# Optimization experiments

Measured on AMD Instinct MI355X. Metric: run time of the kernel, lower is better.

The kernel has to match this reference:

```python
import jax, jax.numpy as jnp
import numpy as np

LAYER_NUM = 2
NUM_CLS = 128
HIDDEN = 256
NUM_NODES = 1024


def setup_inputs() -> dict:
    key = jax.random.key(0)
    ks = jax.random.split(key, 12)
    s = 0.05
    return {
        "x": jax.random.normal(ks[0], (NUM_NODES, HIDDEN), jnp.float32),
        "knowledge": jax.random.uniform(ks[1], (NUM_CLS, NUM_CLS), jnp.float32) / NUM_CLS,
        "w3w": jax.random.normal(ks[2], (HIDDEN, 2 * HIDDEN), jnp.float32) * s,
        "b3w": jax.random.normal(ks[3], (HIDDEN,), jnp.float32) * s,
        "u3": jax.random.normal(ks[4], (HIDDEN, HIDDEN), jnp.float32) * s,
        "bu3": jax.random.normal(ks[5], (HIDDEN,), jnp.float32) * s,
        "w4w": jax.random.normal(ks[6], (HIDDEN, 2 * HIDDEN), jnp.float32) * s,
        "b4w": jax.random.normal(ks[7], (HIDDEN,), jnp.float32) * s,
        "w5w": jax.random.normal(ks[8], (HIDDEN, 2 * HIDDEN), jnp.float32) * s,
        "b5w": jax.random.normal(ks[9], (HIDDEN,), jnp.float32) * s,
        "u5": jax.random.normal(ks[10], (HIDDEN, HIDDEN), jnp.float32) * s,
        "bu5": jax.random.normal(ks[11], (HIDDEN,), jnp.float32) * s,
    }


def reference(x, knowledge, w3w, b3w, u3, bu3, w4w, b4w, w5w, b5w, u5, bu5):
    N, H = x.shape
    C = knowledge.shape[0]
    # hidden[n, c, :] = x[n, :]  (repeat per class)
    hidden = jnp.broadcast_to(x[:, None, :], (N, C, H))
    for _ in range(LAYER_NUM):
        hs = hidden.sum(0)                      # [C, H]
        diff = hs[None, :, :] - hidden          # [N, C, H]
        # knowledge.T @ diff_n  and  knowledge @ diff_n, vectorized over nodes
        left = jnp.einsum('kc,nkh->nch', knowledge, diff)
        right = jnp.einsum('ck,nkh->nch', knowledge, diff)
        av = jnp.concatenate([left, right], axis=-1).reshape(N * C, 2 * H)
        h = hidden.reshape(N * C, H)
        uh3 = h @ u3.T + bu3                    # shared: rv uses fc_eq3_u (source quirk)
        zv = jax.nn.sigmoid(av @ w3w.T + b3w + uh3)
        rv = jax.nn.sigmoid(av @ w4w.T + b4w + uh3)
        hv = jnp.tanh(av @ w5w.T + b5w + (rv * h) @ u5.T + bu5)
        h = (1.0 - zv) * h + zv * hv
        hidden = h.reshape(N, C, H)
    return hidden
```

## Files before the change

kernel.cpp:

```cpp
#include <hip/hip_runtime.h>
#include <cstdint>
#include <cstddef>


#define NODES 1024
#define NCLS  128
#define HID   256

using frag  = __attribute__((ext_vector_type(8))) short;
using frag4 = __attribute__((ext_vector_type(4))) short;
using f32x4 = __attribute__((ext_vector_type(4))) float;

__device__ __forceinline__ float bf2f(unsigned short h){
  unsigned int u = ((unsigned int)h) << 16;
  float f; __builtin_memcpy(&f, &u, 4); return f;
}
__device__ __forceinline__ unsigned short f2bf(float f){
  unsigned int u; __builtin_memcpy(&u, &f, 4);
  u = (u + 0x7fffu + ((u >> 16) & 1u)) >> 16;
  return (unsigned short)u;
}
__device__ __forceinline__ float sigm(float x){ return 1.0f/(1.0f + __expf(-x)); }
__device__ __forceinline__ float tanh_fast(float x){ return 1.0f - 2.0f/(__expf(2.0f*x) + 1.0f); }

#define GLOBAL_AS(p) ((const __attribute__((address_space(1))) void*)(p))
#define LDS_AS(p)    ((__attribute__((address_space(3))) void*)(p))

template<int OUT_BF16>
__global__ __launch_bounds__(256) void gemm_bf16(
    const unsigned short* __restrict__ A0, int ldA0, int K0,
    const unsigned short* __restrict__ A1, int ldA1,
    const unsigned short* __restrict__ BT, int ldB, long bStride,
    void* __restrict__ Cptr, int ldC,
    int Ntiles, int Ktot, unsigned int aMask, int Mtiles)
{
  __shared__ unsigned short As[4096];
  __shared__ unsigned short Bs[4096];
  const int t   = threadIdx.x;
  const int bid = blockIdx.x;
  const int xcd = bid & 7, slot = bid >> 3;
  const int mtPerX = (Mtiles >= 8) ? (Mtiles >> 3) : 1;
  const int mt = xcd * mtPerX + slot / Ntiles;
  const int nt = slot % Ntiles;
  const int lane = t & 63, w = t >> 6;
  const int wm = w >> 1, wn = w & 1;
  const int r = lane & 15, q = lane >> 4;
  const int m0 = mt * 128, n0 = nt * 128;
  const unsigned short* Bbase = BT + (size_t)mt * (size_t)bStride;

  f32x4 acc[4][4] = {};

  for (int kb = 0; kb < Ktot; kb += 32) {
#pragma unroll
    for (int i = 0; i < 2; ++i) {
      int u  = i * 256 + t;
      int mi = u >> 2;
      int kc = (u & 3) * 8;
      int k  = kb + kc;
      const unsigned short* ga;
      if (k < K0) ga = A0 + (size_t)((unsigned int)(m0 + mi) & aMask) * (size_t)ldA0 + k;
      else        ga = A1 + (size_t)(m0 + mi) * (size_t)ldA1 + (k - K0);
      __builtin_amdgcn_global_load_lds(GLOBAL_AS(ga), LDS_AS(&As[u * 8]), 16, 0, 0);
      const unsigned short* gb = Bbase + (size_t)(n0 + mi) * (size_t)ldB + k;
      __builtin_amdgcn_global_load_lds(GLOBAL_AS(gb), LDS_AS(&Bs[u * 8]), 16, 0, 0);
    }
    __syncthreads();

    frag af[4], bf_[4];
#pragma unroll
    for (int x = 0; x < 4; ++x) {
      af[x]  = *(const frag*)&As[(wm * 64 + x * 16 + r) * 32 + q * 8];
      bf_[x] = *(const frag*)&Bs[(wn * 64 + x * 16 + r) * 32 + q * 8];
    }
#pragma unroll
    for (int x = 0; x < 4; ++x)
#pragma unroll
      for (int y = 0; y < 4; ++y)
        acc[x][y] = __builtin_amdgcn_mfma_f32_16x16x32_bf16(af[x], bf_[y], acc[x][y], 0, 0, 0);
    __syncthreads();
  }

#pragma unroll
  for (int x = 0; x < 4; ++x) {
#pragma unroll
    for (int y = 0; y < 4; ++y) {
      int col = n0 + wn * 64 + y * 16 + r;
#pragma unroll
      for (int g = 0; g < 4; ++g) {
        long row = m0 + wm * 64 + x * 16 + q * 4 + g;
        if (OUT_BF16) ((unsigned short*)Cptr)[row * (long)ldC + col] = f2bf(acc[x][y][g]);
        else          ((float*)Cptr)[row * (long)ldC + col] = acc[x][y][g];
      }
    }
  }
}

__global__ __launch_bounds__(256, 4) void gemm_pre(
    const unsigned short* __restrict__ AVH, const unsigned short* __restrict__ H1,
    const unsigned short* __restrict__ WB, unsigned short* __restrict__ PRE)
{
  __shared__ unsigned short As[8192];
  __shared__ unsigned short Bs[8192];
  const int t   = threadIdx.x;
  const int bid = blockIdx.x;
  const int xcd = bid & 7, slot = bid >> 3;
  const int mt = xcd * 128 + slot / 6;
  const int ct = slot % 6;
  const int lane = t & 63, w = t >> 6;
  const int wm = w >> 1, wn = w & 1;
  const int r = lane & 15, q = lane >> 4;
  const int m0 = mt * 128;
  const unsigned short* Wrow = WB + (size_t)(ct * 128) * 768;

  f32x4 acc[4][4] = {};

  for (int kb = 0; kb < 512; kb += 64) {
#pragma unroll
    for (int i = 0; i < 4; ++i) {
      int u  = i * 256 + t;
      int mi = u >> 3;
      int gc = (u & 7) ^ (mi & 7);
      __builtin_amdgcn_global_load_lds(GLOBAL_AS(AVH + (size_t)(m0 + mi) * 512 + kb + gc * 8),
                                       LDS_AS(&As[u * 8]), 16, 0, 0);
      __builtin_amdgcn_global_load_lds(GLOBAL_AS(Wrow + (size_t)mi * 768 + kb + gc * 8),
                                       LDS_AS(&Bs[u * 8]), 16, 0, 0);
    }
    __syncthreads();
#pragma unroll
    for (int kh = 0; kh < 2; ++kh) {
      frag af[4], bf_[4];
#pragma unroll
      for (int x = 0; x < 4; ++x) {
        int ra = wm * 64 + x * 16 + r;
        int rb = wn * 64 + x * 16 + r;
        af[x]  = *(const frag*)&As[ra * 64 + (((kh * 4 + q) ^ (ra & 7)) * 8)];
        bf_[x] = *(const frag*)&Bs[rb * 64 + (((kh * 4 + q) ^ (rb & 7)) * 8)];
      }
#pragma unroll
      for (int x = 0; x < 4; ++x)
#pragma unroll
        for (int y = 0; y < 4; ++y)
          acc[x][y] = __builtin_amdgcn_mfma_f32_16x16x32_bf16(af[x], bf_[y], acc[x][y], 0, 0, 0);
    }
    __syncthreads();
  }

  if (ct < 4) {
    for (int kb = 0; kb < 256; kb += 64) {
#pragma unroll
      for (int i = 0; i < 4; ++i) {
        int u  = i * 256 + t;
        int mi = u >> 3;
        int gc = (u & 7) ^ (mi & 7);
        __builtin_amdgcn_global_load_lds(GLOBAL_AS(H1 + (size_t)(m0 + mi) * 256 + kb + gc * 8),
                                         LDS_AS(&As[u * 8]), 16, 0, 0);
        __builtin_amdgcn_global_load_lds(GLOBAL_AS(Wrow + (size_t)mi * 768 + 512 + kb + gc * 8),
                                         LDS_AS(&Bs[u * 8]), 16, 0, 0);
      }
      __syncthreads();
#pragma unroll
      for (int kh = 0; kh < 2; ++kh) {
        frag af[4], bf_[4];
#pragma unroll
        for (int x = 0; x < 4; ++x) {
          int ra = wm * 64 + x * 16 + r;
          int rb = wn * 64 + x * 16 + r;
          af[x]  = *(const frag*)&As[ra * 64 + (((kh * 4 + q) ^ (ra & 7)) * 8)];
          bf_[x] = *(const frag*)&Bs[rb * 64 + (((kh * 4 + q) ^ (rb & 7)) * 8)];
        }
#pragma unroll
        for (int x = 0; x < 4; ++x)
#pragma unroll
          for (int y = 0; y < 4; ++y)
            acc[x][y] = __builtin_amdgcn_mfma_f32_16x16x32_bf16(af[x], bf_[y], acc[x][y], 0, 0, 0);
      }
      __syncthreads();
    }
  }

#pragma unroll
  for (int x = 0; x < 4; ++x) {
#pragma unroll
    for (int y = 0; y < 4; ++y) {
      int col = ct * 128 + wn * 64 + y * 16 + r;
#pragma unroll
      for (int g = 0; g < 4; ++g) {
        long row = m0 + wm * 64 + x * 16 + q * 4 + g;
        PRE[row * 768 + col] = f2bf(acc[x][y][g]);
      }
    }
  }
}

__global__ __launch_bounds__(256) void gemm_l1(
    const float* __restrict__ XW, const float* __restrict__ SW,
    const float* __restrict__ x,
    const float* __restrict__ b3, const float* __restrict__ b4,
    const float* __restrict__ b5, const float* __restrict__ bu3,
    const float* __restrict__ bu5,
    const float* __restrict__ colsum, const float* __restrict__ rowsum,
    const unsigned short* __restrict__ u5b,
    const unsigned short* __restrict__ KTbN, const unsigned short* __restrict__ KbN,
    unsigned short* __restrict__ H1, unsigned short* __restrict__ AVH)
{
  __shared__ unsigned short SM[17408];
  unsigned short* As = SM;
  unsigned short* Bs = SM + 4096;
  unsigned short* L  = SM;
  __shared__ float tP1[256], tP2[256], tP3[256], tX[256];
  __shared__ float tZ1[256], tZ2[256], tZ3[256];
  __shared__ float tV1[256], tV2[256], tV3[256];
  __shared__ float tCS[128], tRS[128];

  const int t = threadIdx.x, bid = blockIdx.x;
  const int xcd = bid & 7, slot = bid >> 3;
  const int n  = xcd * 128 + (slot >> 1);
  const int nt = slot & 1;
  const int lane = t & 63, w = t >> 6, wm = w >> 1, wn = w & 1;
  const int r = lane & 15, q = lane >> 4;
  const int n0 = nt * 128;
  const float* xw = XW + (size_t)n * 1792;

  {
    int i = t;
    float xwi0 = xw[i], xwi1 = xw[256 + i], xwi2 = xw[512 + i], xwi3 = xw[768 + i];
    float xwi4 = xw[1024 + i], xwi5 = xw[1280 + i], xwu = xw[1536 + i];
    tP1[i] = SW[512 + i] - xwi2;
    tP2[i] = SW[768 + i] - xwi3;
    tP3[i] = xwu + b4[i] + bu3[i];
    tX[i]  = x[(size_t)n * HID + i];
    tZ1[i] = SW[i] - xwi0;
    tZ2[i] = SW[256 + i] - xwi1;
    tZ3[i] = xwu + b3[i] + bu3[i];
    tV1[i] = SW[1024 + i] - xwi4;
    tV2[i] = SW[1280 + i] - xwi5;
    tV3[i] = b5[i] + bu5[i];
    if (t < 128) { tCS[t] = colsum[t]; tRS[t] = rowsum[t]; }
  }
  __syncthreads();

  f32x4 acc[4][4] = {};

  for (int kb = 0; kb < 256; kb += 32) {
#pragma unroll
    for (int i = 0; i < 2; ++i) {
      int u  = i * 256 + t;
      int mi = u >> 2;
      int c  = u & 3;
      int kc = c * 8;
      int k  = kb + kc;
      int gc = c ^ (mi & 3);
      __builtin_amdgcn_global_load_lds(GLOBAL_AS(u5b + (size_t)(n0 + mi) * 256 + kb + gc * 8),
                                       LDS_AS(&Bs[u * 8]), 16, 0, 0);
      float cs = tCS[mi], rs = tRS[mi];
      frag a;
#pragma unroll
      for (int e = 0; e < 8; ++e) {
        int i2 = k + e;
        float pre = cs * tP1[i2] + rs * tP2[i2] + tP3[i2];
        a[e] = (short)f2bf(sigm(pre) * tX[i2]);
      }
      *(frag*)&As[mi * 32 + (c ^ (mi & 3)) * 8] = a;
    }
    __syncthreads();

    frag af[4], bf_[4];
#pragma unroll
    for (int xx = 0; xx < 4; ++xx) {
      int ra = wm * 64 + xx * 16 + r;
      int rb = wn * 64 + xx * 16 + r;
      af[xx]  = *(const frag*)&As[ra * 32 + ((q ^ (ra & 3)) * 8)];
      bf_[xx] = *(const frag*)&Bs[rb * 32 + ((q ^ (rb & 3)) * 8)];
    }
#pragma unroll
    for (int xx = 0; xx < 4; ++xx)
#pragma unroll
      for (int y = 0; y < 4; ++y)
        acc[xx][y] = __builtin_amdgcn_mfma_f32_16x16x32_bf16(af[xx], bf_[y], acc[xx][y], 0, 0, 0);
    __syncthreads();
  }

#pragma unroll
  for (int xx = 0; xx < 4; ++xx) {
#pragma unroll
    for (int y = 0; y < 4; ++y) {
      int j = wn * 64 + y * 16 + r;
      int i = n0 + j;
      frag4 pack;
#pragma unroll
      for (int g = 0; g < 4; ++g) {
        int c = wm * 64 + xx * 16 + q * 4 + g;
        float cs = tCS[c], rs = tRS[c];
        float z  = sigm(cs * tZ1[i] + rs * tZ2[i] + tZ3[i]);
        float p5 = cs * tV1[i] + rs * tV2[i] + tV3[i] + acc[xx][y][g];
        float h1 = (1.0f - z) * tX[i] + z * tanh_fast(p5);
        unsigned short hb = f2bf(h1);
        pack[g] = (short)hb;
        H1[(size_t)(n * 128 + c) * HID + i] = hb;
      }
      *(frag4*)&L[j * 136 + (wm * 64 + xx * 16 + q * 4)] = pack;
    }
  }
  __syncthreads();

#pragma unroll
  for (int s = 0; s < 2; ++s) {
    const unsigned short* Ks = s ? KbN : KTbN;
    f32x4 a2[4][4] = {};
#pragma unroll
    for (int kb = 0; kb < 4; ++kb) {
      frag af[4], bf_[4];
#pragma unroll
      for (int xx = 0; xx < 4; ++xx) {
        int cp = wm * 64 + xx * 16 + r;
        af[xx] = *(const frag*)(Ks + (size_t)cp * 128 + kb * 32 + q * 8);
        int j = wn * 64 + xx * 16 + r;
        bf_[xx] = *(const frag*)&L[j * 136 + kb * 32 + q * 8];
      }
#pragma unroll
      for (int xx = 0; xx < 4; ++xx)
#pragma unroll
        for (int y = 0; y < 4; ++y)
          a2[xx][y] = __builtin_amdgcn_mfma_f32_16x16x32_bf16(af[xx], bf_[y], a2[xx][y], 0, 0, 0);
    }
#pragma unroll
    for (int xx = 0; xx < 4; ++xx)
#pragma unroll
      for (int y = 0; y < 4; ++y) {
        int col = s * 256 + n0 + wn * 64 + y * 16 + r;
#pragma unroll
        for (int g = 0; g < 4; ++g) {
          int cp = wm * 64 + xx * 16 + q * 4 + g;
          AVH[(size_t)(n * 128 + cp) * 512 + col] = f2bf(a2[xx][y][g]);
        }
      }
  }
}

__global__ __launch_bounds__(256) void gemm_l2(
    const unsigned short* __restrict__ PRE, const float* __restrict__ SG,
    const unsigned short* __restrict__ H1, const unsigned short* __restrict__ u5b,
    float* __restrict__ out)
{
  __shared__ unsigned short As[4096], Bs[4096];
  const int t = threadIdx.x, bid = blockIdx.x;
  const int xcd = bid & 7, slot = bid >> 3;
  const int mt = xcd * 128 + (slot >> 1);
  const int nt = slot & 1;
  const int lane = t & 63, w = t >> 6, wm = w >> 1, wn = w & 1;
  const int r = lane & 15, q = lane >> 4;
  const int m0 = mt * 128, n0 = nt * 128;

  f32x4 acc[4][4] = {};

  for (int kb = 0; kb < 256; kb += 32) {
#pragma unroll
    for (int i = 0; i < 2; ++i) {
      int u  = i * 256 + t;
      int mi = u >> 2;
      int c  = u & 3;
      int k  = kb + c * 8;
      int gc = c ^ (mi & 3);
      __builtin_amdgcn_global_load_lds(GLOBAL_AS(u5b + (size_t)(n0 + mi) * 256 + kb + gc * 8),
                                       LDS_AS(&Bs[u * 8]), 16, 0, 0);
      long row = m0 + mi;
      frag p4 = *(const frag*)(PRE + row * 768 + 256 + k);
      frag h1 = *(const frag*)(H1 + row * 256 + k);
      const float* sg = SG + (size_t)mi * 768 + 256 + k;
      frag a;
#pragma unroll
      for (int e = 0; e < 8; ++e) {
        float rv = sigm(sg[e] + bf2f((unsigned short)p4[e]));
        a[e] = (short)f2bf(rv * bf2f((unsigned short)h1[e]));
      }
      *(frag*)&As[mi * 32 + (c ^ (mi & 3)) * 8] = a;
    }
    __syncthreads();

    frag af[4], bf_[4];
#pragma unroll
    for (int xx = 0; xx < 4; ++xx) {
      int ra = wm * 64 + xx * 16 + r;
      int rb = wn * 64 + xx * 16 + r;
      af[xx]  = *(const frag*)&As[ra * 32 + ((q ^ (ra & 3)) * 8)];
      bf_[xx] = *(const frag*)&Bs[rb * 32 + ((q ^ (rb & 3)) * 8)];
    }
#pragma unroll
    for (int xx = 0; xx < 4; ++xx)
#pragma unroll
      for (int y = 0; y < 4; ++y)
        acc[xx][y] = __builtin_amdgcn_mfma_f32_16x16x32_bf16(af[xx], bf_[y], acc[xx][y], 0, 0, 0);
    __syncthreads();
  }

#pragma unroll
  for (int xx = 0; xx < 4; ++xx) {
#pragma unroll
    for (int y = 0; y < 4; ++y) {
      int i = n0 + wn * 64 + y * 16 + r;
#pragma unroll
      for (int g = 0; g < 4; ++g) {
        int c = wm * 64 + xx * 16 + q * 4 + g;
        long row = m0 + c;
        float z  = sigm(SG[(size_t)c * 768 + i] + bf2f(PRE[row * 768 + i]));
        float pv = SG[(size_t)c * 768 + 512 + i] + bf2f(PRE[row * 768 + 512 + i])
                 + acc[xx][y][g];
        float h  = bf2f(H1[row * 256 + i]);
        out[row * 256 + i] = (1.0f - z) * h + z * tanh_fast(pv);
      }
    }
  }
}

__global__ __launch_bounds__(256) void prep_cast(
    const float* __restrict__ x, const float* __restrict__ Kn,
    const float* __restrict__ w3, const float* __restrict__ u3,
    const float* __restrict__ w4, const float* __restrict__ w5,
    const float* __restrict__ u5,
    unsigned short* __restrict__ xb, unsigned short* __restrict__ WB,
    unsigned short* __restrict__ WB2, unsigned short* __restrict__ u5b,
    unsigned short* __restrict__ KbN, unsigned short* __restrict__ KTbN)
{
  int idx = blockIdx.x * 256 + threadIdx.x;
  if (idx < 262144) { xb[idx] = f2bf(x[idx]); return; }
  idx -= 262144;
  if (idx < 589824) {
    int col = idx / 768, j = idx % 768;
    int g = col >> 8, i = col & 255;
    float v;
    if (j < 512) { const float* wg = (g == 0) ? w3 : (g == 1) ? w4 : w5; v = wg[(size_t)i * 512 + j]; }
    else v = (g < 2) ? u3[(size_t)i * 256 + (j - 512)] : 0.0f;
    WB[(size_t)col * 768 + j] = f2bf(v);
    return;
  }
  idx -= 589824;
  if (idx < 458752) {
    int col = idx / 256, h = idx % 256;
    int b = col >> 8, i = col & 255;
    float v = (b < 6) ? ((b < 2 ? w3 : (b < 4 ? w4 : w5))[(size_t)i * 512 + (b & 1) * 256 + h])
                      : u3[(size_t)i * 256 + h];
    WB2[(size_t)col * 256 + h] = f2bf(v);
    return;
  }
  idx -= 458752;
  if (idx < 65536) { u5b[idx] = f2bf(u5[idx]); return; }
  idx -= 65536;
  if (idx < 16384) { int c = idx >> 7, k = idx & 127; KbN[idx]  = f2bf(-Kn[c * 128 + k]); return; }
  idx -= 16384;
  { int c = idx >> 7, k = idx & 127; KTbN[idx] = f2bf(-Kn[k * 128 + c]); }
}

__global__ __launch_bounds__(256) void prep_reduce(
    const float* __restrict__ x, const float* __restrict__ Kn,
    float* __restrict__ S, float* __restrict__ colsum, float* __restrict__ rowsum)
{
  int b = blockIdx.x, t = threadIdx.x;
  if (b < 8) {
    float s = 0.f;
    for (int n = 0; n < 128; ++n) s += x[(size_t)(b * 128 + n) * HID + t];
    atomicAdd(&S[t], s);
  } else if (b == 8) {
    if (t < NCLS) { float s = 0.f; for (int k = 0; k < NCLS; ++k) s += Kn[k * NCLS + t]; colsum[t] = s; }
  } else {
    if (t < NCLS) { float s = 0.f; for (int k = 0; k < NCLS; ++k) s += Kn[t * NCLS + k]; rowsum[t] = s; }
  }
}

__global__ __launch_bounds__(256) void prep_sw(
    const float* __restrict__ S, const float* __restrict__ w3,
    const float* __restrict__ w4, const float* __restrict__ w5, float* __restrict__ SW)
{
  int col = blockIdx.x * 256 + threadIdx.x;
  int b = col >> 8, i = col & 255;
  const float* w = (b < 2) ? w3 : (b < 4) ? w4 : w5;
  const float* row = w + (size_t)i * 512 + (b & 1) * 256;
  float s = 0.f;
  for (int h = 0; h < HID; ++h) s += S[h] * row[h];
  SW[col] = s;
}

__global__ __launch_bounds__(256) void reduce_hs(
    const unsigned short* __restrict__ H1, float* __restrict__ hs)
{
  int bid = blockIdx.x;
  int c = bid >> 5, nch = bid & 31;
  int i = threadIdx.x;
  const unsigned short* p = H1 + (size_t)nch * 32 * NCLS * HID + (size_t)c * HID + i;
  float s = 0.f;
  for (int n = 0; n < 32; ++n) s += bf2f(p[(size_t)n * NCLS * HID]);
  atomicAdd(&hs[c * HID + i], s);
}

__global__ __launch_bounds__(256) void p2a(
    const float* __restrict__ hs, const float* __restrict__ w3,
    const float* __restrict__ w4, const float* __restrict__ w5, float* __restrict__ hsW)
{
  __shared__ float hrow[HID];
  int k = blockIdx.x & 127, b = blockIdx.x >> 7;
  int t = threadIdx.x;
  hrow[t] = hs[k * HID + t];
  __syncthreads();
  const float* w = (b < 2) ? w3 : (b < 4) ? w4 : w5;
  const float* row = w + (size_t)t * 512 + (b & 1) * 256;
  float s = 0.f;
  for (int h = 0; h < HID; ++h) s += hrow[h] * row[h];
  hsW[(size_t)k * 1536 + b * 256 + t] = s;
}

__global__ __launch_bounds__(256) void p2b(
    const float* __restrict__ hsW, const float* __restrict__ Kn,
    const float* __restrict__ b3, const float* __restrict__ b4, const float* __restrict__ b5,
    const float* __restrict__ bu3, const float* __restrict__ bu5, float* __restrict__ SG)
{
  __shared__ float kc[NCLS], kr[NCLS];
  int c = blockIdx.x, t = threadIdx.x;
  if (t < NCLS) { kc[t] = Kn[t * NCLS + c]; kr[t] = Kn[c * NCLS + t]; }
  __syncthreads();
  for (int g = 0; g < 3; ++g) {
    int i = t;
    const float* L = hsW + (size_t)(2 * g) * 256 + i;
    const float* R = hsW + (size_t)(2 * g + 1) * 256 + i;
    float s = 0.f;
    for (int k = 0; k < NCLS; ++k) s += kc[k] * L[(size_t)k * 1536] + kr[k] * R[(size_t)k * 1536];
    const float* bg = (g == 0) ? b3 : (g == 1) ? b4 : b5;
    s += bg[i] + ((g < 2) ? bu3[i] : bu5[i]);
    SG[(size_t)c * 768 + g * 256 + i] = s;
  }
}

extern "C" void kernel_launch(void* const* d_in, const int* in_sizes, int n_in,
                              void* d_out, int out_size, void* d_ws, size_t ws_size,
                              hipStream_t stream) {
  (void)in_sizes; (void)n_in; (void)out_size; (void)ws_size;
  const float* x   = (const float*)d_in[0];
  const float* Kn  = (const float*)d_in[1];
  const float* w3  = (const float*)d_in[2];
  const float* b3  = (const float*)d_in[3];
  const float* u3  = (const float*)d_in[4];
  const float* bu3 = (const float*)d_in[5];
  const float* w4  = (const float*)d_in[6];
  const float* b4  = (const float*)d_in[7];
  const float* w5  = (const float*)d_in[8];
  const float* b5  = (const float*)d_in[9];
  const float* u5  = (const float*)d_in[10];
  const float* bu5 = (const float*)d_in[11];
  float* out = (float*)d_out;

  char* w = (char*)d_ws;
  unsigned short* AVH = (unsigned short*)(w);
  unsigned short* PRE = (unsigned short*)(w + 134217728);
  unsigned short* H1  = (unsigned short*)(w + 335544320);
  float*          XW  = (float*)(w + 402653184);
  char* misc = w + 409993216;
  float* S      = (float*)(misc);
  float* hs     = (float*)(misc + 1024);
  float* SW     = (float*)(misc + 132096);
  float* colsum = (float*)(misc + 138240);
  float* rowsum = (float*)(misc + 138752);
  float* hsW    = (float*)(misc + 139264);
  float* SG     = (float*)(misc + 925696);
  unsigned short* WB   = (unsigned short*)(misc + 1318912);
  unsigned short* WB2  = (unsigned short*)(misc + 2498560);
  unsigned short* u5b  = (unsigned short*)(misc + 3416064);
  unsigned short* KbN  = (unsigned short*)(misc + 3547136);
  unsigned short* KTbN = (unsigned short*)(misc + 3579904);
  unsigned short* xb   = (unsigned short*)(misc + 3612672);

  hipMemsetAsync(misc, 0, 132096, stream);

  prep_cast<<<5504, 256, 0, stream>>>(x, Kn, w3, u3, w4, w5, u5, xb, WB, WB2, u5b, KbN, KTbN);
  prep_reduce<<<10, 256, 0, stream>>>(x, Kn, S, colsum, rowsum);
  prep_sw<<<6, 256, 0, stream>>>(S, w3, w4, w5, SW);

  gemm_bf16<0><<<8 * 14, 256, 0, stream>>>(xb, 256, 256, xb, 256, WB2, 256, 0L,
                                           (void*)XW, 1792, 14, 256, 0xFFFFFFFFu, 8);
  gemm_l1<<<2048, 256, 0, stream>>>(XW, SW, x, b3, b4, b5, bu3, bu5,
                                    colsum, rowsum, u5b, KTbN, KbN, H1, AVH);

  reduce_hs<<<4096, 256, 0, stream>>>(H1, hs);
  p2a<<<768, 256, 0, stream>>>(hs, w3, w4, w5, hsW);
  p2b<<<128, 256, 0, stream>>>(hsW, Kn, b3, b4, b5, bu3, bu5, SG);

  gemm_pre<<<6144, 256, 0, stream>>>(AVH, H1, WB, PRE);

  gemm_l2<<<2048, 256, 0, stream>>>(PRE, SG, H1, u5b, out);
}
```

Before: 776.5 us.

## Fuse reset-gate product into gemm_pre epilogue and stage stores through LDS

The gemm_pre epilogue now computes rv*h for the reset-gate column tiles and writes the bf16 result into PRE, so gemm_l2 can stream its A operand directly with global_load_lds using a K step of 64 instead of computing sigmoids in its load loop. Both kernels now stage output tiles through swizzled shared memory so the global writes are coalesced 16-byte stores, where before each element was stored individually. gemm_l2 also gains a launch_bounds occupancy hint and a larger shared buffer. The tradeoff is extra syncs and LDS traffic in the epilogues, plus extra SG and H1 reads inside gemm_pre.

```diff
diff --git a/kernel.cpp b/kernel.cpp
--- a/kernel.cpp
+++ b/kernel.cpp
@@ -97,10 +97,12 @@
 
 __global__ __launch_bounds__(256, 4) void gemm_pre(
     const unsigned short* __restrict__ AVH, const unsigned short* __restrict__ H1,
-    const unsigned short* __restrict__ WB, unsigned short* __restrict__ PRE)
-{
-  __shared__ unsigned short As[8192];
-  __shared__ unsigned short Bs[8192];
+    const unsigned short* __restrict__ WB, const float* __restrict__ SG,
+    unsigned short* __restrict__ PRE)
+{
+  __shared__ unsigned short SM[16384];
+  unsigned short* As = SM;
+  unsigned short* Bs = SM + 8192;
   const int t   = threadIdx.x;
   const int bid = blockIdx.x;
   const int xcd = bid & 7, slot = bid >> 3;
@@ -178,17 +180,35 @@
     }
   }
 
-#pragma unroll
-  for (int x = 0; x < 4; ++x) {
-#pragma unroll
-    for (int y = 0; y < 4; ++y) {
-      int col = ct * 128 + wn * 64 + y * 16 + r;
-#pragma unroll
-      for (int g = 0; g < 4; ++g) {
-        long row = m0 + wm * 64 + x * 16 + q * 4 + g;
-        PRE[row * 768 + col] = f2bf(acc[x][y][g]);
-      }
-    }
+  {
+    const int isR = (ct == 2 || ct == 3);
+    const int ih0 = (ct - 2) * 128;
+#pragma unroll
+    for (int x = 0; x < 4; ++x)
+#pragma unroll
+      for (int y = 0; y < 4; ++y) {
+        int lc = wn * 64 + y * 16 + r;
+#pragma unroll
+        for (int g = 0; g < 4; ++g) {
+          int cr = wm * 64 + x * 16 + q * 4 + g;
+          float v = acc[x][y][g];
+          if (isR) {
+            int i = ih0 + lc;
+            float sg4 = SG[(size_t)cr * 768 + 256 + i];
+            float h1v = bf2f(H1[(size_t)(m0 + cr) * 256 + i]);
+            v = sigm(sg4 + v) * h1v;
+          }
+          SM[cr * 128 + (((lc >> 3) ^ (cr & 7)) * 8) + (lc & 7)] = f2bf(v);
+        }
+      }
+  }
+  __syncthreads();
+#pragma unroll
+  for (int it = 0; it < 8; ++it) {
+    int u = it * 256 + t;
+    int rr = u >> 4, cc = u & 15;
+    frag v = *(const frag*)&SM[rr * 128 + ((cc ^ (rr & 7)) * 8)];
+    *(frag*)&PRE[(size_t)(m0 + rr) * 768 + ct * 128 + cc * 8] = v;
   }
 }
 
@@ -337,12 +357,15 @@
   }
 }
 
-__global__ __launch_bounds__(256) void gemm_l2(
+__global__ __launch_bounds__(256, 4) void gemm_l2(
     const unsigned short* __restrict__ PRE, const float* __restrict__ SG,
     const unsigned short* __restrict__ H1, const unsigned short* __restrict__ u5b,
     float* __restrict__ out)
 {
-  __shared__ unsigned short As[4096], Bs[4096];
+  __shared__ unsigned short SM[16384];
+  unsigned short* As = SM;
+  unsigned short* Bs = SM + 8192;
+  float* F = (float*)SM;
   const int t = threadIdx.x, bid = blockIdx.x;
   const int xcd = bid & 7, slot = bid >> 3;
   const int mt = xcd * 128 + (slot >> 1);
@@ -350,65 +373,73 @@
   const int lane = t & 63, w = t >> 6, wm = w >> 1, wn = w & 1;
   const int r = lane & 15, q = lane >> 4;
   const int m0 = mt * 128, n0 = nt * 128;
+  const unsigned short* RH = PRE + 256;
 
   f32x4 acc[4][4] = {};
 
-  for (int kb = 0; kb < 256; kb += 32) {
-#pragma unroll
-    for (int i = 0; i < 2; ++i) {
+  for (int kb = 0; kb < 256; kb += 64) {
+#pragma unroll
+    for (int i = 0; i < 4; ++i) {
       int u  = i * 256 + t;
-      int mi = u >> 2;
-      int c  = u & 3;
-      int k  = kb + c * 8;
-      int gc = c ^ (mi & 3);
+      int mi = u >> 3;
+      int gc = (u & 7) ^ (mi & 7);
+      __builtin_amdgcn_global_load_lds(GLOBAL_AS(RH + (size_t)(m0 + mi) * 768 + kb + gc * 8),
+                                       LDS_AS(&As[u * 8]), 16, 0, 0);
       __builtin_amdgcn_global_load_lds(GLOBAL_AS(u5b + (size_t)(n0 + mi) * 256 + kb + gc * 8),
                                        LDS_AS(&Bs[u * 8]), 16, 0, 0);
-      long row = m0 + mi;
-      frag p4 = *(const frag*)(PRE + row * 768 + 256 + k);
-      frag h1 = *(const frag*)(H1 + row * 256 + k);
-      const float* sg = SG + (size_t)mi * 768 + 256 + k;
-      frag a;
-#pragma unroll
-      for (int e = 0; e < 8; ++e) {
-        float rv = sigm(sg[e] + bf2f((unsigned short)p4[e]));
-        a[e] = (short)f2bf(rv * bf2f((unsigned short)h1[e]));
-      }
-      *(frag*)&As[mi * 32 + (c ^ (mi & 3)) * 8] = a;
-    }
-    __syncthreads();
-
-    frag af[4], bf_[4];
-#pragma unroll
-    for (int xx = 0; xx < 4; ++xx) {
-      int ra = wm * 64 + xx * 16 + r;
-      int rb = wn * 64 + xx * 16 + r;
-      af[xx]  = *(const frag*)&As[ra * 32 + ((q ^ (ra & 3)) * 8)];
-      bf_[xx] = *(const frag*)&Bs[rb * 32 + ((q ^ (rb & 3)) * 8)];
-    }
-#pragma unroll
-    for (int xx = 0; xx < 4; ++xx)
-#pragma unroll
-      for (int y = 0; y < 4; ++y)
-        acc[xx][y] = __builtin_amdgcn_mfma_f32_16x16x32_bf16(af[xx], bf_[y], acc[xx][y], 0, 0, 0);
-    __syncthreads();
-  }
-
-#pragma unroll
-  for (int xx = 0; xx < 4; ++xx) {
-#pragma unroll
-    for (int y = 0; y < 4; ++y) {
-      int i = n0 + wn * 64 + y * 16 + r;
-#pragma unroll
-      for (int g = 0; g < 4; ++g) {
-        int c = wm * 64 + xx * 16 + q * 4 + g;
-        long row = m0 + c;
-        float z  = sigm(SG[(size_t)c * 768 + i] + bf2f(PRE[row * 768 + i]));
-        float pv = SG[(size_t)c * 768 + 512 + i] + bf2f(PRE[row * 768 + 512 + i])
-                 + acc[xx][y][g];
-        float h  = bf2f(H1[row * 256 + i]);
-        out[row * 256 + i] = (1.0f - z) * h + z * tanh_fast(pv);
-      }
-    }
+    }
+    __syncthreads();
+#pragma unroll
+    for (int kh = 0; kh < 2; ++kh) {
+      frag af[4], bf_[4];
+#pragma unroll
+      for (int x = 0; x < 4; ++x) {
+        int ra = wm * 64 + x * 16 + r;
+        int rb = wn * 64 + x * 16 + r;
+        af[x]  = *(const frag*)&As[ra * 64 + (((kh * 4 + q) ^ (ra & 7)) * 8)];
+        bf_[x] = *(const frag*)&Bs[rb * 64 + (((kh * 4 + q) ^ (rb & 7)) * 8)];
+      }
+#pragma unroll
+      for (int x = 0; x < 4; ++x)
+#pragma unroll
+        for (int y = 0; y < 4; ++y)
+          acc[x][y] = __builtin_amdgcn_mfma_f32_16x16x32_bf16(af[x], bf_[y], acc[x][y], 0, 0, 0);
+    }
+    __syncthreads();
+  }
+
+  for (int ch = 0; ch < 2; ++ch) {
+    if (wm == ch) {
+#pragma unroll
+      for (int x = 0; x < 4; ++x)
+#pragma unroll
+        for (int y = 0; y < 4; ++y) {
+          int lc = wn * 64 + y * 16 + r;
+          int i  = n0 + lc;
+#pragma unroll
+          for (int g = 0; g < 4; ++g) {
+            int lrow = x * 16 + q * 4 + g;
+            int c = ch * 64 + lrow;
+            long row = m0 + c;
+            float z  = sigm(SG[(size_t)c * 768 + i] + bf2f(PRE[row * 768 + i]));
+            float pv = SG[(size_t)c * 768 + 512 + i] + bf2f(PRE[row * 768 + 512 + i])
+                     + acc[x][y][g];
+            float h  = bf2f(H1[row * 256 + i]);
+            F[lrow * 128 + (lc ^ (((lrow >> 2) & 1) << 4))] =
+                (1.0f - z) * h + z * tanh_fast(pv);
+          }
+        }
+    }
+    __syncthreads();
+#pragma unroll
+    for (int it = 0; it < 8; ++it) {
+      int u = it * 256 + t;
+      int rr = u >> 5, xc = u & 31;
+      int pc = (xc * 4) ^ (((rr >> 2) & 1) << 4);
+      f32x4 v = *(const f32x4*)&F[rr * 128 + pc];
+      *(f32x4*)&out[(size_t)(m0 + ch * 64 + rr) * 256 + n0 + xc * 4] = v;
+    }
+    __syncthreads();
   }
 }
 
@@ -581,7 +612,7 @@
   p2a<<<768, 256, 0, stream>>>(hs, w3, w4, w5, hsW);
   p2b<<<128, 256, 0, stream>>>(hsW, Kn, b3, b4, b5, bu3, bu5, SG);
 
-  gemm_pre<<<6144, 256, 0, stream>>>(AVH, H1, WB, PRE);
+  gemm_pre<<<6144, 256, 0, stream>>>(AVH, H1, WB, SG, PRE);
 
   gemm_l2<<<2048, 256, 0, stream>>>(PRE, SG, H1, u5b, out);
 }
```

After: 1.111 ms. 43.1% more time.
